# Kernel optimization log

Hardware: AMD Instinct MI355X
Metric: run time of the kernel (lower is better)

The kernel has to match this reference:

```python
import jax, jax.numpy as jnp
import numpy as np

NUM_HEADS = 64
NUM_KV_HEADS = 8
HEAD_DIM = 128
Q_MULT = NUM_HEADS // NUM_KV_HEADS  # 8
CACHE_LEN = 8192
SLIDING_WINDOW = 4096
BATCH = 16
SM_SCALE = 1.0 / float(np.sqrt(HEAD_DIM))


def setup_inputs() -> dict:
    key = jax.random.key(0)
    k1, k2, k3, k4, k5 = jax.random.split(key, 5)
    return {
        "Q": jax.random.normal(k1, (BATCH, 1, NUM_HEADS * HEAD_DIM), dtype=jnp.float32),
        "K": jax.random.normal(k2, (BATCH, 1, NUM_KV_HEADS * HEAD_DIM), dtype=jnp.float32),
        "V": jax.random.normal(k3, (BATCH, 1, NUM_KV_HEADS * HEAD_DIM), dtype=jnp.float32),
        "K_cache": jax.random.normal(k4, (BATCH, CACHE_LEN, NUM_KV_HEADS * HEAD_DIM), dtype=jnp.float32),
        "V_cache": jax.random.normal(k5, (BATCH, CACHE_LEN, NUM_KV_HEADS * HEAD_DIM), dtype=jnp.float32),
        "sinks": jnp.zeros((NUM_HEADS,), dtype=jnp.float32),
    }


def reference(Q, K, V, K_cache, V_cache, sinks):
    B = Q.shape[0]
    total_len = CACHE_LEN + 1
    # reshape to (B, kv_heads, q_mult, d) / (B, len, kv_heads, d)
    q = Q.reshape(B, NUM_KV_HEADS, Q_MULT, HEAD_DIM)
    k_new = K.reshape(B, 1, NUM_KV_HEADS, HEAD_DIM)
    v_new = V.reshape(B, 1, NUM_KV_HEADS, HEAD_DIM)
    k_full = jnp.concatenate([K_cache.reshape(B, CACHE_LEN, NUM_KV_HEADS, HEAD_DIM), k_new], axis=1)
    v_full = jnp.concatenate([V_cache.reshape(B, CACHE_LEN, NUM_KV_HEADS, HEAD_DIM), v_new], axis=1)

    # scores: (B, kv_heads, q_mult, total_len) -- GQA: each kv head serves q_mult query heads
    qk = jnp.einsum("bhmd,bkhd->bhmk", q, k_full) * SM_SCALE

    # sliding-window mask (static shapes: total_len > window here)
    if SLIDING_WINDOW > 0 and total_len > SLIDING_WINDOW:
        pos = jnp.arange(total_len)
        qk = jnp.where(pos[None, None, None, :] < total_len - SLIDING_WINDOW, -jnp.inf, qk)

    # append sink logit per query head, softmax, then drop sink column
    s = sinks.reshape(1, NUM_KV_HEADS, Q_MULT, 1)
    logits = jnp.concatenate([qk, jnp.broadcast_to(s, (B, NUM_KV_HEADS, Q_MULT, 1))], axis=-1)
    w = jax.nn.softmax(logits, axis=-1)[..., :-1]

    attn = jnp.einsum("bhmk,bkhd->bhmd", w, v_full)
    return attn.reshape(B, 1, NUM_HEADS * HEAD_DIM)
```

## Files before the change

kernel.cpp:

```cpp
#include <hip/hip_runtime.h>
#include <math.h>

#define BATCH 16
#define KVH 8
#define QM 8
#define NH 64
#define HD 128
#define CACHE 8192
#define WIN 4096
#define TOTAL (CACHE + 1)
#define PSTART (TOTAL - WIN)
#define TILE 64
#define KSTRIDE (KVH * HD)
#define LDSTR 132
#define REC_FLOATS (QM * (HD + 2))

template <int NC>
__global__ __launch_bounds__(256, 4)
void attn_partial(const float* __restrict__ Q,
                  const float* __restrict__ Knew,
                  const float* __restrict__ Vnew,
                  const float* __restrict__ Kc,
                  const float* __restrict__ Vc,
                  float* __restrict__ ws) {
    constexpr int CL = WIN / NC;
    const int c   = blockIdx.x;
    const int kvh = blockIdx.y;
    const int b   = blockIdx.z;
    const int t   = threadIdx.x;

    __shared__ float q_s[QM][HD];
    __shared__ float kv_s[TILE][LDSTR];
    __shared__ float w_s[QM][TILE];

    {
        const float* qp = Q + ((size_t)b * NH + kvh * QM) * HD;
        for (int i = t; i < QM * HD; i += 256)
            q_s[i / HD][i % HD] = qp[i] * 0.08838834764831845f;
    }
    __syncthreads();

    const int h  = t >> 5;
    const int lp = t & 31;

    float acc0 = 0.f, acc1 = 0.f, acc2 = 0.f, acc3 = 0.f;
    float m_run = -INFINITY;
    float l_run = 0.f;

    const size_t cache_base = (size_t)b * CACHE * KSTRIDE + (size_t)kvh * HD;
    const size_t new_base   = (size_t)b * KSTRIDE + (size_t)kvh * HD;
    const int p_base = PSTART + c * CL;

    for (int tb = 0; tb < CL; tb += TILE) {
        for (int i = t; i < TILE * (HD / 4); i += 256) {
            int r = i >> 5;
            int g = i & 31;
            int p = p_base + tb + r;
            const float* src = (p < CACHE) ? (Kc + cache_base + (size_t)p * KSTRIDE)
                                           : (Knew + new_base);
            float4 v = *reinterpret_cast<const float4*>(src + g * 4);
            *reinterpret_cast<float4*>(&kv_s[r][g * 4]) = v;
        }
        __syncthreads();

        float s0 = 0.f, s1 = 0.f;
        {
            const float* qrow = q_s[h];
            const float* k0 = kv_s[lp];
            const float* k1 = kv_s[lp + 32];
            #pragma unroll
            for (int d = 0; d < HD; d += 4) {
                float4 qv  = *reinterpret_cast<const float4*>(qrow + d);
                float4 kv0 = *reinterpret_cast<const float4*>(k0 + d);
                float4 kv1 = *reinterpret_cast<const float4*>(k1 + d);
                s0 += qv.x * kv0.x + qv.y * kv0.y + qv.z * kv0.z + qv.w * kv0.w;
                s1 += qv.x * kv1.x + qv.y * kv1.y + qv.z * kv1.z + qv.w * kv1.w;
            }
        }

        float mt = fmaxf(s0, s1);
        #pragma unroll
        for (int off = 16; off; off >>= 1) mt = fmaxf(mt, __shfl_xor(mt, off));
        float m_new = fmaxf(m_run, mt);
        float e0 = __expf(s0 - m_new);
        float e1 = __expf(s1 - m_new);
        float rs = __expf(m_run - m_new);
        float lsum = e0 + e1;
        #pragma unroll
        for (int off = 16; off; off >>= 1) lsum += __shfl_xor(lsum, off);
        l_run = l_run * rs + lsum;
        m_run = m_new;
        acc0 *= rs; acc1 *= rs; acc2 *= rs; acc3 *= rs;
        w_s[h][lp]      = e0;
        w_s[h][lp + 32] = e1;
        __syncthreads();

        for (int i = t; i < TILE * (HD / 4); i += 256) {
            int r = i >> 5;
            int g = i & 31;
            int p = p_base + tb + r;
            const float* src = (p < CACHE) ? (Vc + cache_base + (size_t)p * KSTRIDE)
                                           : (Vnew + new_base);
            float4 v = *reinterpret_cast<const float4*>(src + g * 4);
            *reinterpret_cast<float4*>(&kv_s[r][g * 4]) = v;
        }
        __syncthreads();

        #pragma unroll 4
        for (int p = 0; p < TILE; ++p) {
            float wv = w_s[h][p];
            acc0 += wv * kv_s[p][lp];
            acc1 += wv * kv_s[p][lp + 32];
            acc2 += wv * kv_s[p][lp + 64];
            acc3 += wv * kv_s[p][lp + 96];
        }
        __syncthreads();
    }

    float* rec = ws + (size_t)((b * KVH + kvh) * NC + c) * REC_FLOATS;
    if (lp == 0) { rec[h] = m_run; rec[QM + h] = l_run; }
    float* accp = rec + 2 * QM + h * HD;
    accp[lp]      = acc0;
    accp[lp + 32] = acc1;
    accp[lp + 64] = acc2;
    accp[lp + 96] = acc3;
}

template <int NC>
__global__ __launch_bounds__(256)
void attn_combine(const float* __restrict__ ws,
                  const float* __restrict__ sinks,
                  float* __restrict__ out) {
    const int kvh = blockIdx.x;
    const int b   = blockIdx.y;
    const int t   = threadIdx.x;
    const int h   = t >> 5;
    const int lp  = t & 31;

    const float* base = ws + (size_t)((b * KVH + kvh) * NC) * REC_FLOATS;
    const float sk = sinks[kvh * QM + h];

    float m[NC], l[NC];
    float M = sk;
    #pragma unroll
    for (int c = 0; c < NC; ++c) {
        m[c] = base[(size_t)c * REC_FLOATS + h];
        l[c] = base[(size_t)c * REC_FLOATS + QM + h];
        M = fmaxf(M, m[c]);
    }
    float denom = __expf(sk - M);
    float wgt[NC];
    #pragma unroll
    for (int c = 0; c < NC; ++c) {
        wgt[c] = __expf(m[c] - M);
        denom += wgt[c] * l[c];
    }
    float inv = 1.f / denom;

    float o0 = 0.f, o1 = 0.f, o2 = 0.f, o3 = 0.f;
    #pragma unroll
    for (int c = 0; c < NC; ++c) {
        const float* accp = base + (size_t)c * REC_FLOATS + 2 * QM + h * HD;
        o0 += wgt[c] * accp[lp];
        o1 += wgt[c] * accp[lp + 32];
        o2 += wgt[c] * accp[lp + 64];
        o3 += wgt[c] * accp[lp + 96];
    }
    float* op = out + (size_t)b * NH * HD + (size_t)(kvh * QM + h) * HD;
    op[lp]      = o0 * inv;
    op[lp + 32] = o1 * inv;
    op[lp + 64] = o2 * inv;
    op[lp + 96] = o3 * inv;
}

template <int NC>
static void launch_nc(const float* Q, const float* K, const float* V,
                      const float* Kc, const float* Vc, const float* sinks,
                      float* out, float* ws, hipStream_t stream) {
    dim3 g1(NC, KVH, BATCH);
    attn_partial<NC><<<g1, 256, 0, stream>>>(Q, K, V, Kc, Vc, ws);
    dim3 g2(KVH, BATCH);
    attn_combine<NC><<<g2, 256, 0, stream>>>(ws, sinks, out);
}

extern "C" void kernel_launch(void* const* d_in, const int* in_sizes, int n_in,
                              void* d_out, int out_size, void* d_ws, size_t ws_size,
                              hipStream_t stream) {
    const float* Q     = (const float*)d_in[0];
    const float* K     = (const float*)d_in[1];
    const float* V     = (const float*)d_in[2];
    const float* Kc    = (const float*)d_in[3];
    const float* Vc    = (const float*)d_in[4];
    const float* sinks = (const float*)d_in[5];
    float* out = (float*)d_out;
    float* ws  = (float*)d_ws;

    auto need = [](int nc) {
        return (size_t)BATCH * KVH * nc * REC_FLOATS * sizeof(float);
    };
    if (ws_size >= need(8))      launch_nc<8>(Q, K, V, Kc, Vc, sinks, out, ws, stream);
    else if (ws_size >= need(4)) launch_nc<4>(Q, K, V, Kc, Vc, sinks, out, ws, stream);
    else if (ws_size >= need(2)) launch_nc<2>(Q, K, V, Kc, Vc, sinks, out, ws, stream);
    else                         launch_nc<1>(Q, K, V, Kc, Vc, sinks, out, ws, stream);
}
```

Measured before the change: 121.2 us.

## Rewrite decode attention as register-resident, all-heads-per-block streaming kernel

Each block now covers all 8 KV heads of one batch for one position span. Each thread holds a float4 slice of K/V per position in registers, with Q for 8 query heads kept in registers, so shared-memory tiling and block barriers are gone. Scores are reduced with a transpose-style shuffle tree, and the online-softmax rescale is skipped unless the max grows by more than 8. Splits rise to 64 with a pairwise streaming combine, and the edge-position branch is specialized. Costs are higher register pressure, many small workspace records, and lazy rescaling that allows exponents up to e^8 before renormalizing.

New measurement: 122.0 us. No clear change (+0.7%).

```diff
diff --git a/kernel.cpp b/kernel.cpp
--- a/kernel.cpp
+++ b/kernel.cpp
@@ -8,179 +8,196 @@
 #define HD 128
 #define CACHE 8192
 #define WIN 4096
-#define TOTAL (CACHE + 1)
-#define PSTART (TOTAL - WIN)
-#define TILE 64
+#define PSTART (CACHE + 1 - WIN)
 #define KSTRIDE (KVH * HD)
-#define LDSTR 132
-#define REC_FLOATS (QM * (HD + 2))
-
-template <int NC>
+#define REC_FLOATS (2 * QM + QM * HD)
+#define SM_SCALE 0.08838834764831845f
+
+#define BCAST(x, imm) __int_as_float(__builtin_amdgcn_ds_swizzle(__float_as_int(x), (imm)))
+
+#define SCALE_ACC(h, rr) { acc[h].x *= rr; acc[h].y *= rr; acc[h].z *= rr; acc[h].w *= rr; }
+#define PV_ACC(h, ww)    { acc[h].x += ww*vc4.x; acc[h].y += ww*vc4.y; acc[h].z += ww*vc4.z; acc[h].w += ww*vc4.w; }
+
+template <int NSPLIT, bool EDGE>
+__device__ __forceinline__ void attn_body(
+    int c, int b, int t,
+    const float* __restrict__ Q, const float* __restrict__ Knew,
+    const float* __restrict__ Vnew, const float* __restrict__ Kc,
+    const float* __restrict__ Vc, float* __restrict__ ws) {
+    constexpr int SPAN = WIN / NSPLIT;
+    static_assert(SPAN % 2 == 0, "unroll-2");
+    const int g  = t >> 5;
+    const int dp = t & 31;
+    const int pb = PSTART + c * SPAN;
+
+    float4 q4[8];
+    {
+        const float* qp = Q + ((size_t)b * NH + (size_t)g * QM) * HD + dp * 4;
+        #pragma unroll
+        for (int h = 0; h < 8; ++h) {
+            float4 v = *reinterpret_cast<const float4*>(qp + h * HD);
+            q4[h] = make_float4(v.x * SM_SCALE, v.y * SM_SCALE,
+                                v.z * SM_SCALE, v.w * SM_SCALE);
+        }
+    }
+
+    const float* kb_ = Kc + ((size_t)b * CACHE + pb) * KSTRIDE + t * 4;
+    const float* vb_ = Vc + ((size_t)b * CACHE + pb) * KSTRIDE + t * 4;
+    const float* kn_ = Knew + (size_t)b * KSTRIDE + t * 4;
+    const float* vn_ = Vnew + (size_t)b * KSTRIDE + t * 4;
+
+    auto LK = [&](int j) -> float4 {
+        const float* a = kb_ + (size_t)j * KSTRIDE;
+        if (EDGE && (pb + j >= CACHE)) a = kn_;
+        return *reinterpret_cast<const float4*>(a);
+    };
+    auto LV = [&](int j) -> float4 {
+        const float* a = vb_ + (size_t)j * KSTRIDE;
+        if (EDGE && (pb + j >= CACHE)) a = vn_;
+        return *reinterpret_cast<const float4*>(a);
+    };
+
+    float4 acc[8];
+    #pragma unroll
+    for (int h = 0; h < 8; ++h) acc[h] = make_float4(0.f, 0.f, 0.f, 0.f);
+    float mrun = -INFINITY, lrun = 0.f;
+
+    auto STEP = [&](float4 kc4, float4 vc4) {
+        float p0 = q4[0].x*kc4.x + q4[0].y*kc4.y + q4[0].z*kc4.z + q4[0].w*kc4.w;
+        float p1 = q4[1].x*kc4.x + q4[1].y*kc4.y + q4[1].z*kc4.z + q4[1].w*kc4.w;
+        float p2 = q4[2].x*kc4.x + q4[2].y*kc4.y + q4[2].z*kc4.z + q4[2].w*kc4.w;
+        float p3 = q4[3].x*kc4.x + q4[3].y*kc4.y + q4[3].z*kc4.z + q4[3].w*kc4.w;
+        float p4 = q4[4].x*kc4.x + q4[4].y*kc4.y + q4[4].z*kc4.z + q4[4].w*kc4.w;
+        float p5 = q4[5].x*kc4.x + q4[5].y*kc4.y + q4[5].z*kc4.z + q4[5].w*kc4.w;
+        float p6 = q4[6].x*kc4.x + q4[6].y*kc4.y + q4[6].z*kc4.z + q4[6].w*kc4.w;
+        float p7 = q4[7].x*kc4.x + q4[7].y*kc4.y + q4[7].z*kc4.z + q4[7].w*kc4.w;
+        const bool s1 = dp & 1;
+        float a0 = (s1?p1:p0) + __shfl_xor((s1?p0:p1), 1);
+        float a1 = (s1?p3:p2) + __shfl_xor((s1?p2:p3), 1);
+        float a2 = (s1?p5:p4) + __shfl_xor((s1?p4:p5), 1);
+        float a3 = (s1?p7:p6) + __shfl_xor((s1?p6:p7), 1);
+        const bool s2 = dp & 2;
+        float b0 = (s2?a1:a0) + __shfl_xor((s2?a0:a1), 2);
+        float b1 = (s2?a3:a2) + __shfl_xor((s2?a2:a3), 2);
+        const bool s4 = dp & 4;
+        float s = (s4?b1:b0) + __shfl_xor((s4?b0:b1), 4);
+        s += __shfl_xor(s, 8);
+        s += __shfl_xor(s, 16);
+
+        if (__any(s > mrun + 8.0f)) {
+            float mn = fmaxf(mrun, s);
+            float rs = __expf(mrun - mn);
+            mrun = mn; lrun *= rs;
+            float r0 = BCAST(rs, 0x00); SCALE_ACC(0, r0);
+            float r1 = BCAST(rs, 0x20); SCALE_ACC(1, r1);
+            float r2 = BCAST(rs, 0x40); SCALE_ACC(2, r2);
+            float r3 = BCAST(rs, 0x60); SCALE_ACC(3, r3);
+            float r4 = BCAST(rs, 0x80); SCALE_ACC(4, r4);
+            float r5 = BCAST(rs, 0xA0); SCALE_ACC(5, r5);
+            float r6 = BCAST(rs, 0xC0); SCALE_ACC(6, r6);
+            float r7 = BCAST(rs, 0xE0); SCALE_ACC(7, r7);
+        }
+        float e = __expf(s - mrun);
+        lrun += e;
+        float w0 = BCAST(e, 0x00); PV_ACC(0, w0);
+        float w1 = BCAST(e, 0x20); PV_ACC(1, w1);
+        float w2 = BCAST(e, 0x40); PV_ACC(2, w2);
+        float w3 = BCAST(e, 0x60); PV_ACC(3, w3);
+        float w4 = BCAST(e, 0x80); PV_ACC(4, w4);
+        float w5 = BCAST(e, 0xA0); PV_ACC(5, w5);
+        float w6 = BCAST(e, 0xC0); PV_ACC(6, w6);
+        float w7 = BCAST(e, 0xE0); PV_ACC(7, w7);
+    };
+
+    float4 ka = LK(0), va = LV(0), kb4 = LK(1), vb4 = LV(1);
+    for (int j = 0; j < SPAN; j += 2) {
+        float4 k0 = ka, v0 = va;
+        ka = LK(j + 2); va = LV(j + 2);
+        STEP(k0, v0);
+        float4 k1 = kb4, v1 = vb4;
+        kb4 = LK(j + 3); vb4 = LV(j + 3);
+        STEP(k1, v1);
+    }
+
+    float* rec = ws + ((size_t)(b * KVH + g) * NSPLIT + c) * REC_FLOATS;
+    if (dp < 8) { rec[dp] = mrun; rec[QM + dp] = lrun; }
+    #pragma unroll
+    for (int h = 0; h < 8; ++h)
+        *reinterpret_cast<float4*>(rec + 2 * QM + h * HD + dp * 4) = acc[h];
+}
+
+template <int NSPLIT>
 __global__ __launch_bounds__(256, 4)
-void attn_partial(const float* __restrict__ Q,
-                  const float* __restrict__ Knew,
-                  const float* __restrict__ Vnew,
-                  const float* __restrict__ Kc,
-                  const float* __restrict__ Vc,
-                  float* __restrict__ ws) {
-    constexpr int CL = WIN / NC;
-    const int c   = blockIdx.x;
-    const int kvh = blockIdx.y;
-    const int b   = blockIdx.z;
-    const int t   = threadIdx.x;
-
-    __shared__ float q_s[QM][HD];
-    __shared__ float kv_s[TILE][LDSTR];
-    __shared__ float w_s[QM][TILE];
-
-    {
-        const float* qp = Q + ((size_t)b * NH + kvh * QM) * HD;
-        for (int i = t; i < QM * HD; i += 256)
-            q_s[i / HD][i % HD] = qp[i] * 0.08838834764831845f;
-    }
-    __syncthreads();
-
-    const int h  = t >> 5;
-    const int lp = t & 31;
-
-    float acc0 = 0.f, acc1 = 0.f, acc2 = 0.f, acc3 = 0.f;
-    float m_run = -INFINITY;
-    float l_run = 0.f;
-
-    const size_t cache_base = (size_t)b * CACHE * KSTRIDE + (size_t)kvh * HD;
-    const size_t new_base   = (size_t)b * KSTRIDE + (size_t)kvh * HD;
-    const int p_base = PSTART + c * CL;
-
-    for (int tb = 0; tb < CL; tb += TILE) {
-        for (int i = t; i < TILE * (HD / 4); i += 256) {
-            int r = i >> 5;
-            int g = i & 31;
-            int p = p_base + tb + r;
-            const float* src = (p < CACHE) ? (Kc + cache_base + (size_t)p * KSTRIDE)
-                                           : (Knew + new_base);
-            float4 v = *reinterpret_cast<const float4*>(src + g * 4);
-            *reinterpret_cast<float4*>(&kv_s[r][g * 4]) = v;
-        }
-        __syncthreads();
-
-        float s0 = 0.f, s1 = 0.f;
-        {
-            const float* qrow = q_s[h];
-            const float* k0 = kv_s[lp];
-            const float* k1 = kv_s[lp + 32];
-            #pragma unroll
-            for (int d = 0; d < HD; d += 4) {
-                float4 qv  = *reinterpret_cast<const float4*>(qrow + d);
-                float4 kv0 = *reinterpret_cast<const float4*>(k0 + d);
-                float4 kv1 = *reinterpret_cast<const float4*>(k1 + d);
-                s0 += qv.x * kv0.x + qv.y * kv0.y + qv.z * kv0.z + qv.w * kv0.w;
-                s1 += qv.x * kv1.x + qv.y * kv1.y + qv.z * kv1.z + qv.w * kv1.w;
-            }
-        }
-
-        float mt = fmaxf(s0, s1);
-        #pragma unroll
-        for (int off = 16; off; off >>= 1) mt = fmaxf(mt, __shfl_xor(mt, off));
-        float m_new = fmaxf(m_run, mt);
-        float e0 = __expf(s0 - m_new);
-        float e1 = __expf(s1 - m_new);
-        float rs = __expf(m_run - m_new);
-        float lsum = e0 + e1;
-        #pragma unroll
-        for (int off = 16; off; off >>= 1) lsum += __shfl_xor(lsum, off);
-        l_run = l_run * rs + lsum;
-        m_run = m_new;
-        acc0 *= rs; acc1 *= rs; acc2 *= rs; acc3 *= rs;
-        w_s[h][lp]      = e0;
-        w_s[h][lp + 32] = e1;
-        __syncthreads();
-
-        for (int i = t; i < TILE * (HD / 4); i += 256) {
-            int r = i >> 5;
-            int g = i & 31;
-            int p = p_base + tb + r;
-            const float* src = (p < CACHE) ? (Vc + cache_base + (size_t)p * KSTRIDE)
-                                           : (Vnew + new_base);
-            float4 v = *reinterpret_cast<const float4*>(src + g * 4);
-            *reinterpret_cast<float4*>(&kv_s[r][g * 4]) = v;
-        }
-        __syncthreads();
-
-        #pragma unroll 4
-        for (int p = 0; p < TILE; ++p) {
-            float wv = w_s[h][p];
-            acc0 += wv * kv_s[p][lp];
-            acc1 += wv * kv_s[p][lp + 32];
-            acc2 += wv * kv_s[p][lp + 64];
-            acc3 += wv * kv_s[p][lp + 96];
-        }
-        __syncthreads();
-    }
-
-    float* rec = ws + (size_t)((b * KVH + kvh) * NC + c) * REC_FLOATS;
-    if (lp == 0) { rec[h] = m_run; rec[QM + h] = l_run; }
-    float* accp = rec + 2 * QM + h * HD;
-    accp[lp]      = acc0;
-    accp[lp + 32] = acc1;
-    accp[lp + 64] = acc2;
-    accp[lp + 96] = acc3;
+void attn_partial(const float* __restrict__ Q, const float* __restrict__ Knew,
+                  const float* __restrict__ Vnew, const float* __restrict__ Kc,
+                  const float* __restrict__ Vc, float* __restrict__ ws) {
+    const int c = blockIdx.x, b = blockIdx.y, t = threadIdx.x;
+    if (c == NSPLIT - 1)
+        attn_body<NSPLIT, true >(c, b, t, Q, Knew, Vnew, Kc, Vc, ws);
+    else
+        attn_body<NSPLIT, false>(c, b, t, Q, Knew, Vnew, Kc, Vc, ws);
 }
 
 template <int NC>
 __global__ __launch_bounds__(256)
-void attn_combine(const float* __restrict__ ws,
-                  const float* __restrict__ sinks,
+void attn_combine(const float* __restrict__ ws, const float* __restrict__ sinks,
                   float* __restrict__ out) {
-    const int kvh = blockIdx.x;
-    const int b   = blockIdx.y;
-    const int t   = threadIdx.x;
-    const int h   = t >> 5;
-    const int lp  = t & 31;
-
-    const float* base = ws + (size_t)((b * KVH + kvh) * NC) * REC_FLOATS;
+    const int kvh = blockIdx.x, b = blockIdx.y, t = threadIdx.x;
+    const int h = t >> 5, lp = t & 31;
+    const float* base = ws + (size_t)(b * KVH + kvh) * NC * REC_FLOATS;
+
+    float M0 = -INFINITY, d0 = 0.f, M1 = -INFINITY, d1 = 0.f;
+    float4 o0 = make_float4(0.f, 0.f, 0.f, 0.f);
+    float4 o1 = make_float4(0.f, 0.f, 0.f, 0.f);
+
+    #pragma unroll 2
+    for (int cc = 0; cc < NC; cc += 2) {
+        {
+            const float* rec = base + (size_t)cc * REC_FLOATS;
+            float mc = rec[h], lc = rec[QM + h];
+            float4 a = *reinterpret_cast<const float4*>(rec + 2*QM + h*HD + 4*lp);
+            float Mn = fmaxf(M0, mc);
+            float fo = __expf(M0 - Mn), fc = __expf(mc - Mn);
+            d0 = d0 * fo + fc * lc;
+            o0.x = o0.x*fo + fc*a.x; o0.y = o0.y*fo + fc*a.y;
+            o0.z = o0.z*fo + fc*a.z; o0.w = o0.w*fo + fc*a.w;
+            M0 = Mn;
+        }
+        {
+            const float* rec = base + (size_t)(cc + 1) * REC_FLOATS;
+            float mc = rec[h], lc = rec[QM + h];
+            float4 a = *reinterpret_cast<const float4*>(rec + 2*QM + h*HD + 4*lp);
+            float Mn = fmaxf(M1, mc);
+            float fo = __expf(M1 - Mn), fc = __expf(mc - Mn);
+            d1 = d1 * fo + fc * lc;
+            o1.x = o1.x*fo + fc*a.x; o1.y = o1.y*fo + fc*a.y;
+            o1.z = o1.z*fo + fc*a.z; o1.w = o1.w*fo + fc*a.w;
+            M1 = Mn;
+        }
+    }
+
     const float sk = sinks[kvh * QM + h];
-
-    float m[NC], l[NC];
-    float M = sk;
-    #pragma unroll
-    for (int c = 0; c < NC; ++c) {
-        m[c] = base[(size_t)c * REC_FLOATS + h];
-        l[c] = base[(size_t)c * REC_FLOATS + QM + h];
-        M = fmaxf(M, m[c]);
-    }
-    float denom = __expf(sk - M);
-    float wgt[NC];
-    #pragma unroll
-    for (int c = 0; c < NC; ++c) {
-        wgt[c] = __expf(m[c] - M);
-        denom += wgt[c] * l[c];
-    }
-    float inv = 1.f / denom;
-
-    float o0 = 0.f, o1 = 0.f, o2 = 0.f, o3 = 0.f;
-    #pragma unroll
-    for (int c = 0; c < NC; ++c) {
-        const float* accp = base + (size_t)c * REC_FLOATS + 2 * QM + h * HD;
-        o0 += wgt[c] * accp[lp];
-        o1 += wgt[c] * accp[lp + 32];
-        o2 += wgt[c] * accp[lp + 64];
-        o3 += wgt[c] * accp[lp + 96];
-    }
-    float* op = out + (size_t)b * NH * HD + (size_t)(kvh * QM + h) * HD;
-    op[lp]      = o0 * inv;
-    op[lp + 32] = o1 * inv;
-    op[lp + 64] = o2 * inv;
-    op[lp + 96] = o3 * inv;
-}
-
-template <int NC>
+    float M = fmaxf(fmaxf(M0, M1), sk);
+    float f0 = __expf(M0 - M), f1 = __expf(M1 - M);
+    float d = d0 * f0 + d1 * f1 + __expf(sk - M);
+    float inv = 1.f / d;
+    float4 r;
+    r.x = (o0.x*f0 + o1.x*f1) * inv;
+    r.y = (o0.y*f0 + o1.y*f1) * inv;
+    r.z = (o0.z*f0 + o1.z*f1) * inv;
+    r.w = (o0.w*f0 + o1.w*f1) * inv;
+    float* op = out + (size_t)b * NH * HD + (size_t)(kvh * QM + h) * HD + 4 * lp;
+    *reinterpret_cast<float4*>(op) = r;
+}
+
+template <int NSPLIT>
 static void launch_nc(const float* Q, const float* K, const float* V,
                       const float* Kc, const float* Vc, const float* sinks,
                       float* out, float* ws, hipStream_t stream) {
-    dim3 g1(NC, KVH, BATCH);
-    attn_partial<NC><<<g1, 256, 0, stream>>>(Q, K, V, Kc, Vc, ws);
+    dim3 g1(NSPLIT, BATCH);
+    attn_partial<NSPLIT><<<g1, 256, 0, stream>>>(Q, K, V, Kc, Vc, ws);
     dim3 g2(KVH, BATCH);
-    attn_combine<NC><<<g2, 256, 0, stream>>>(ws, sinks, out);
+    attn_combine<NSPLIT><<<g2, 256, 0, stream>>>(ws, sinks, out);
 }
 
 extern "C" void kernel_launch(void* const* d_in, const int* in_sizes, int n_in,
@@ -198,8 +215,7 @@
     auto need = [](int nc) {
         return (size_t)BATCH * KVH * nc * REC_FLOATS * sizeof(float);
     };
-    if (ws_size >= need(8))      launch_nc<8>(Q, K, V, Kc, Vc, sinks, out, ws, stream);
-    else if (ws_size >= need(4)) launch_nc<4>(Q, K, V, Kc, Vc, sinks, out, ws, stream);
-    else if (ws_size >= need(2)) launch_nc<2>(Q, K, V, Kc, Vc, sinks, out, ws, stream);
-    else                         launch_nc<1>(Q, K, V, Kc, Vc, sinks, out, ws, stream);
-}
+    if (ws_size >= need(64))      launch_nc<64>(Q, K, V, Kc, Vc, sinks, out, ws, stream);
+    else if (ws_size >= need(32)) launch_nc<32>(Q, K, V, Kc, Vc, sinks, out, ws, stream);
+    else                          launch_nc<16>(Q, K, V, Kc, Vc, sinks, out, ws, stream);
+}
```
